# Performance work log

Hardware: AMD Instinct MI355X
Metric: run time of the kernel (lower is better)

Reference implementation:

```python
import jax, jax.numpy as jnp
import numpy as np

B, F, E, T = 4, 128, 3000, 6000  # batch, features, input edges, unroll_target


def setup_inputs() -> dict:
    key = jax.random.key(0)
    k1, k2 = jax.random.split(key)
    features = jax.random.normal(k1, (B, F, E), dtype=jnp.float32)
    # Sparse one-hot-like group matrix: each padded group matrix is binary with
    # a few nonzeros per target column (as produced by mesh.get_groups + pad_groups).
    unroll_mat = (jax.random.uniform(k2, (B, E, T)) < (2.0 / E)).astype(jnp.float32)
    # occurrences[b, t] = number of times target edge t occurs across groups;
    # pad_occurrences pads with 1, so clamp to a minimum of 1.
    occurrences = jnp.maximum(unroll_mat.sum(axis=1), 1.0)  # (B, T)
    return {"features": features, "unroll_mat": unroll_mat, "occurrences": occurrences}


def reference(features, unroll_mat, occurrences):
    # unroll_mat: (B, E, T) padded group matrix; occurrences: (B, T)
    # normalized mapping, then dense bmm: (B,F,E) @ (B,E,T) -> (B,F,T)
    norm_mat = unroll_mat / occurrences[:, None, :]
    return jnp.einsum('bfe,bet->bft', features, norm_mat)
```

## Files before the change

kernel.cpp:

```cpp
#include <hip/hip_runtime.h>

#define B 4
#define F 128
#define E 3000
#define T 6000
#define BN 48
#define KSTEP 32
#define NKT 94
#define NTT 125
#define ESLOT 40

typedef float f32x4 __attribute__((ext_vector_type(4)));
typedef short bf16x8 __attribute__((ext_vector_type(8)));

static __device__ __forceinline__ unsigned short f32_bf16(float x) {
    unsigned u = __float_as_uint(x);
    u += 0x7FFFu + ((u >> 16) & 1u);
    return (unsigned short)(u >> 16);
}

__global__ __launch_bounds__(256) void build_afrag(const float* __restrict__ feat,
                                                   unsigned short* __restrict__ afrag) {
    const int gid = blockIdx.x * 256 + threadIdx.x;
    if (gid >= B * NKT * 8 * 64) return;
    const int lane = gid & 63;
    const int frag = gid >> 6;
    const int ft = frag & 7;
    const int kt = (frag >> 3) % NKT;
    const int b  = frag / (8 * NKT);
    const int m  = ft * 16 + (lane & 15);
    const int k0 = kt * 32 + (lane >> 4) * 8;
    const float* src = feat + ((size_t)b * F + m) * E;
    unsigned short v[8];
#pragma unroll
    for (int j = 0; j < 8; ++j) {
        const int k = k0 + j;
        v[j] = (k < E) ? f32_bf16(src[k]) : (unsigned short)0;
    }
    uint4 pack;
    pack.x = (unsigned)v[0] | ((unsigned)v[1] << 16);
    pack.y = (unsigned)v[2] | ((unsigned)v[3] << 16);
    pack.z = (unsigned)v[4] | ((unsigned)v[5] << 16);
    pack.w = (unsigned)v[6] | ((unsigned)v[7] << 16);
    *reinterpret_cast<uint4*>(afrag + (size_t)frag * 512 + lane * 8) = pack;
}

__global__ __launch_bounds__(256, 2) void unpool_mfma_ws(
        const float* __restrict__ unroll,
        const unsigned short* __restrict__ afrag,
        const float* __restrict__ occ,
        float* __restrict__ out) {
    __shared__ unsigned short ut[4][2][BN * ESLOT];
    __shared__ f32x4 red[2][3][3][64];

    const int nwg  = NTT * B;
    const int orig = blockIdx.x + gridDim.x * blockIdx.y;
    const int q = nwg / 8, r = nwg % 8;
    const int xcd = orig & 7, lin = orig >> 3;
    const int newid = (xcd < r ? xcd * (q + 1) : r * (q + 1) + (xcd - r) * q) + lin;
    const int tb = newid % NTT;
    const int b  = newid / NTT;
    const int t0 = tb * BN;

    const int tid  = threadIdx.x;
    const int lane = tid & 63;
    const int w    = tid >> 6;
    const int lrow = lane & 15;
    const int g    = lane >> 4;

    const float* ub = unroll + (size_t)b * E * T + t0;
    const unsigned short* ab = afrag + (size_t)b * NKT * 8 * 512;
    unsigned short (*myut)[BN * ESLOT] = ut[w];

    int e_l[6], t4_l[6];
#pragma unroll
    for (int j = 0; j < 6; ++j) {
        const int idx = lane + 64 * j;
        e_l[j]  = idx / 12;
        t4_l[j] = (idx % 12) * 4;
    }

    const int s0 = w * 23 + (w < 2 ? w : 2);
    const int ns = 23 + (w < 2 ? 1 : 0);

    f32x4 acc[8][3] = {};

#define ULOAD(DST, S)                                                                  \
    { _Pragma("unroll") for (int j = 0; j < 6; ++j) {                                  \
          const int e = (S) * KSTEP + e_l[j];                                          \
          DST[j] = (e < E) ? *reinterpret_cast<const float4*>(ub + (size_t)e * T + t4_l[j]) \
                           : make_float4(0.0f, 0.0f, 0.0f, 0.0f); } }

#define UWRITE(SRC, BUF)                                                               \
    { _Pragma("unroll") for (int j = 0; j < 6; ++j) {                                  \
          unsigned short* p = &myut[BUF][e_l[j]];                                      \
          p[(t4_l[j] + 0) * ESLOT] = (__float_as_uint(SRC[j].x) != 0u) ? 0x3F80u : 0u; \
          p[(t4_l[j] + 1) * ESLOT] = (__float_as_uint(SRC[j].y) != 0u) ? 0x3F80u : 0u; \
          p[(t4_l[j] + 2) * ESLOT] = (__float_as_uint(SRC[j].z) != 0u) ? 0x3F80u : 0u; \
          p[(t4_l[j] + 3) * ESLOT] = (__float_as_uint(SRC[j].w) != 0u) ? 0x3F80u : 0u; } }

#define STEP(S, BUF, UVOLD, UVNEW)                                                     \
    {                                                                                  \
        bf16x8 afr[8];                                                                 \
        const unsigned short* ap = ab + (size_t)(S) * 8 * 512 + lane * 8;              \
        _Pragma("unroll") for (int ft = 0; ft < 8; ++ft)                               \
            afr[ft] = *reinterpret_cast<const bf16x8*>(ap + ft * 512);                 \
        __builtin_amdgcn_sched_barrier(0);                                             \
        if ((S) + 2 < s0 + ns) ULOAD(UVNEW, (S) + 2);                                  \
        const bf16x8 bf0 = *reinterpret_cast<const bf16x8*>(&myut[BUF][(0 * 16 + lrow) * ESLOT + 8 * g]); \
        const bf16x8 bf1 = *reinterpret_cast<const bf16x8*>(&myut[BUF][(1 * 16 + lrow) * ESLOT + 8 * g]); \
        const bf16x8 bf2 = *reinterpret_cast<const bf16x8*>(&myut[BUF][(2 * 16 + lrow) * ESLOT + 8 * g]); \
        _Pragma("unroll") for (int ft = 0; ft < 8; ++ft) {                             \
            acc[ft][0] = __builtin_amdgcn_mfma_f32_16x16x32_bf16(afr[ft], bf0, acc[ft][0], 0, 0, 0); \
            acc[ft][1] = __builtin_amdgcn_mfma_f32_16x16x32_bf16(afr[ft], bf1, acc[ft][1], 0, 0, 0); \
            acc[ft][2] = __builtin_amdgcn_mfma_f32_16x16x32_bf16(afr[ft], bf2, acc[ft][2], 0, 0, 0); } \
        if ((S) + 1 < s0 + ns) UWRITE(UVOLD, (BUF) ^ 1);                               \
    }

    float4 uvA[6], uvB[6];
    ULOAD(uvA, s0);
    UWRITE(uvA, 0);
    if (ns > 1) ULOAD(uvA, s0 + 1);

    for (int i = 0; i < ns; i += 2) {
        STEP(s0 + i, 0, uvA, uvB);
        if (i + 1 < ns) STEP(s0 + i + 1, 1, uvB, uvA);
    }
#undef STEP
#undef UWRITE
#undef ULOAD

    float inv[3];
#pragma unroll
    for (int nt = 0; nt < 3; ++nt)
        inv[nt] = 1.0f / occ[b * T + t0 + nt * 16 + lrow];
    float* ob = out + (size_t)b * F * T;

#pragma unroll
    for (int p = 0; p < 4; ++p) {
        __syncthreads();
#pragma unroll
        for (int c = 0; c < 2; ++c) {
            const int ft = 2 * p + c;
            const int fw = 2 * c + (p & 1);
            if (w != fw) {
                const int slot = (w - fw + 4) % 4 - 1;
#pragma unroll
                for (int nt = 0; nt < 3; ++nt)
                    red[c][slot][nt][lane] = acc[ft][nt];
            }
        }
        __syncthreads();
#pragma unroll
        for (int c = 0; c < 2; ++c) {
            const int ft = 2 * p + c;
            const int fw = 2 * c + (p & 1);
            if (w == fw) {
#pragma unroll
                for (int nt = 0; nt < 3; ++nt) {
                    f32x4 v = acc[ft][nt];
#pragma unroll
                    for (int sI = 0; sI < 3; ++sI) v += red[c][sI][nt][lane];
                    const int t = t0 + nt * 16 + lrow;
#pragma unroll
                    for (int rr = 0; rr < 4; ++rr) {
                        const int f = ft * 16 + g * 4 + rr;
                        __builtin_nontemporal_store(v[rr] * inv[nt], ob + (size_t)f * T + t);
                    }
                }
            }
        }
    }
}

__global__ void unpool_dense_fallback(const float* __restrict__ features,
                                      const float* __restrict__ unroll,
                                      const float* __restrict__ occ,
                                      float* __restrict__ out) {
    const int b = blockIdx.z;
    const int f = blockIdx.y;
    const int t = blockIdx.x * 64 + threadIdx.x;
    if (t >= T) return;
    const float* frow = features + ((size_t)b * F + f) * E;
    const float* ubp = unroll + (size_t)b * E * T;
    float acc = 0.0f;
    for (int e = 0; e < E; ++e) acc += frow[e] * ubp[(size_t)e * T + t];
    out[((size_t)b * F + f) * T + t] = acc / occ[b * T + t];
}

extern "C" void kernel_launch(void* const* d_in, const int* in_sizes, int n_in,
                              void* d_out, int out_size, void* d_ws, size_t ws_size,
                              hipStream_t stream) {
    const float* features = (const float*)d_in[0];
    const float* unroll   = (const float*)d_in[1];
    const float* occ      = (const float*)d_in[2];
    float* out = (float*)d_out;

    const size_t afrag_bytes = (size_t)B * NKT * 8 * 512 * sizeof(unsigned short);
    if (ws_size < afrag_bytes) {
        dim3 g((T + 63) / 64, F, B);
        unpool_dense_fallback<<<g, 64, 0, stream>>>(features, unroll, occ, out);
        return;
    }

    unsigned short* afrag = (unsigned short*)d_ws;

    const int nthr = B * NKT * 8 * 64;
    build_afrag<<<(nthr + 255) / 256, 256, 0, stream>>>(features, afrag);

    unpool_mfma_ws<<<dim3(NTT, B), 256, 0, stream>>>(unroll, afrag, occ, out);
}
```

Measured before the change: 74.90 us.

## Bit-pack unroll matrix in a pre-pass and expand bits to bf16 in the GEMM

Adds a pre-pass kernel that reads the full fp32 unroll matrix once and writes it as 64-bit ballot bitmasks, one bit per entry. The main MFMA kernel then reads these compact bitmasks instead of fp32 data and rebuilds the bf16 B fragments in registers by shifting and masking. This drops the LDS staging buffers and the transpose writes. The full 288MB fp32 read still happens, now in the separate bitpack kernel, so the gain depends on that streaming pass running near full bandwidth. It also adds a kernel launch and scattered 4-byte bitmask gathers in the GEMM.

```diff
diff --git a/kernel.cpp b/kernel.cpp
--- a/kernel.cpp
+++ b/kernel.cpp
@@ -8,7 +8,8 @@
 #define KSTEP 32
 #define NKT 94
 #define NTT 125
-#define ESLOT 40
+#define RQW 96
+#define RDW 192
 
 typedef float f32x4 __attribute__((ext_vector_type(4)));
 typedef short bf16x8 __attribute__((ext_vector_type(8)));
@@ -45,19 +46,43 @@
     *reinterpret_cast<uint4*>(afrag + (size_t)frag * 512 + lane * 8) = pack;
 }
 
-__global__ __launch_bounds__(256, 2) void unpool_mfma_ws(
-        const float* __restrict__ unroll,
+__global__ __launch_bounds__(256) void bitpack(const float* __restrict__ unroll,
+                                               unsigned long long* __restrict__ bitmask) {
+    const int rid  = blockIdx.x * 4 + (threadIdx.x >> 6);
+    const int lane = threadIdx.x & 63;
+    const float* row = unroll + (size_t)rid * T;
+    unsigned long long* orow = bitmask + (size_t)rid * RQW;
+
+#pragma unroll
+    for (int ch = 0; ch < 24; ++ch) {
+        float4 v = make_float4(0.0f, 0.0f, 0.0f, 0.0f);
+        if (ch < 23 || lane < 28)
+            v = *reinterpret_cast<const float4*>(row + ch * 256 + lane * 4);
+        const unsigned long long b0 = __ballot(v.x != 0.0f);
+        const unsigned long long b1 = __ballot(v.y != 0.0f);
+        const unsigned long long b2 = __ballot(v.z != 0.0f);
+        const unsigned long long b3 = __ballot(v.w != 0.0f);
+        if (lane == 0) {
+            orow[ch * 4 + 0] = b0;
+            orow[ch * 4 + 1] = b1;
+            orow[ch * 4 + 2] = b2;
+            orow[ch * 4 + 3] = b3;
+        }
+    }
+}
+
+__global__ __launch_bounds__(256, 2) void unpool_mfma_bits(
+        const unsigned* __restrict__ bm,
         const unsigned short* __restrict__ afrag,
         const float* __restrict__ occ,
         float* __restrict__ out) {
-    __shared__ unsigned short ut[4][2][BN * ESLOT];
     __shared__ f32x4 red[2][3][3][64];
 
     const int nwg  = NTT * B;
     const int orig = blockIdx.x + gridDim.x * blockIdx.y;
-    const int q = nwg / 8, r = nwg % 8;
+    const int q_ = nwg / 8, r_ = nwg % 8;
     const int xcd = orig & 7, lin = orig >> 3;
-    const int newid = (xcd < r ? xcd * (q + 1) : r * (q + 1) + (xcd - r) * q) + lin;
+    const int newid = (xcd < r_ ? xcd * (q_ + 1) : r_ * (q_ + 1) + (xcd - r_) * q_) + lin;
     const int tb = newid % NTT;
     const int b  = newid / NTT;
     const int t0 = tb * BN;
@@ -68,67 +93,59 @@
     const int lrow = lane & 15;
     const int g    = lane >> 4;
 
-    const float* ub = unroll + (size_t)b * E * T + t0;
     const unsigned short* ab = afrag + (size_t)b * NKT * 8 * 512;
-    unsigned short (*myut)[BN * ESLOT] = ut[w];
-
-    int e_l[6], t4_l[6];
-#pragma unroll
-    for (int j = 0; j < 6; ++j) {
-        const int idx = lane + 64 * j;
-        e_l[j]  = idx / 12;
-        t4_l[j] = (idx % 12) * 4;
+    const unsigned* bmb = bm + (size_t)b * E * RDW;
+
+    int C[3], sh[3];
+#pragma unroll
+    for (int nt = 0; nt < 3; ++nt) {
+        const int t = t0 + nt * 16 + lrow;
+        C[nt]  = (t >> 8) * 8 + (t & 3) * 2 + ((t >> 7) & 1);
+        sh[nt] = (t >> 2) & 31;
     }
 
     const int s0 = w * 23 + (w < 2 ? w : 2);
-    const int ns = 23 + (w < 2 ? 1 : 0);
+    const int send = s0 + 23 + (w < 2 ? 1 : 0);
 
     f32x4 acc[8][3] = {};
 
-#define ULOAD(DST, S)                                                                  \
-    { _Pragma("unroll") for (int j = 0; j < 6; ++j) {                                  \
-          const int e = (S) * KSTEP + e_l[j];                                          \
-          DST[j] = (e < E) ? *reinterpret_cast<const float4*>(ub + (size_t)e * T + t4_l[j]) \
-                           : make_float4(0.0f, 0.0f, 0.0f, 0.0f); } }
-
-#define UWRITE(SRC, BUF)                                                               \
-    { _Pragma("unroll") for (int j = 0; j < 6; ++j) {                                  \
-          unsigned short* p = &myut[BUF][e_l[j]];                                      \
-          p[(t4_l[j] + 0) * ESLOT] = (__float_as_uint(SRC[j].x) != 0u) ? 0x3F80u : 0u; \
-          p[(t4_l[j] + 1) * ESLOT] = (__float_as_uint(SRC[j].y) != 0u) ? 0x3F80u : 0u; \
-          p[(t4_l[j] + 2) * ESLOT] = (__float_as_uint(SRC[j].z) != 0u) ? 0x3F80u : 0u; \
-          p[(t4_l[j] + 3) * ESLOT] = (__float_as_uint(SRC[j].w) != 0u) ? 0x3F80u : 0u; } }
-
-#define STEP(S, BUF, UVOLD, UVNEW)                                                     \
-    {                                                                                  \
-        bf16x8 afr[8];                                                                 \
-        const unsigned short* ap = ab + (size_t)(S) * 8 * 512 + lane * 8;              \
-        _Pragma("unroll") for (int ft = 0; ft < 8; ++ft)                               \
-            afr[ft] = *reinterpret_cast<const bf16x8*>(ap + ft * 512);                 \
-        __builtin_amdgcn_sched_barrier(0);                                             \
-        if ((S) + 2 < s0 + ns) ULOAD(UVNEW, (S) + 2);                                  \
-        const bf16x8 bf0 = *reinterpret_cast<const bf16x8*>(&myut[BUF][(0 * 16 + lrow) * ESLOT + 8 * g]); \
-        const bf16x8 bf1 = *reinterpret_cast<const bf16x8*>(&myut[BUF][(1 * 16 + lrow) * ESLOT + 8 * g]); \
-        const bf16x8 bf2 = *reinterpret_cast<const bf16x8*>(&myut[BUF][(2 * 16 + lrow) * ESLOT + 8 * g]); \
-        _Pragma("unroll") for (int ft = 0; ft < 8; ++ft) {                             \
-            acc[ft][0] = __builtin_amdgcn_mfma_f32_16x16x32_bf16(afr[ft], bf0, acc[ft][0], 0, 0, 0); \
-            acc[ft][1] = __builtin_amdgcn_mfma_f32_16x16x32_bf16(afr[ft], bf1, acc[ft][1], 0, 0, 0); \
-            acc[ft][2] = __builtin_amdgcn_mfma_f32_16x16x32_bf16(afr[ft], bf2, acc[ft][2], 0, 0, 0); } \
-        if ((S) + 1 < s0 + ns) UWRITE(UVOLD, (BUF) ^ 1);                               \
-    }
-
-    float4 uvA[6], uvB[6];
-    ULOAD(uvA, s0);
-    UWRITE(uvA, 0);
-    if (ns > 1) ULOAD(uvA, s0 + 1);
-
-    for (int i = 0; i < ns; i += 2) {
-        STEP(s0 + i, 0, uvA, uvB);
-        if (i + 1 < ns) STEP(s0 + i + 1, 1, uvB, uvA);
-    }
-#undef STEP
-#undef UWRITE
-#undef ULOAD
+    for (int s = s0; s < send; ++s) {
+        unsigned q[3][8];
+        const unsigned* rp = bmb + (size_t)(32 * s + 8 * g) * RDW;
+#pragma unroll
+        for (int nt = 0; nt < 3; ++nt)
+#pragma unroll
+            for (int j = 0; j < 8; ++j)
+                q[nt][j] = rp[j * RDW + C[nt]];
+
+        bf16x8 afr[8];
+        const unsigned short* ap = ab + (size_t)s * 8 * 512 + lane * 8;
+#pragma unroll
+        for (int ft = 0; ft < 8; ++ft)
+            afr[ft] = *reinterpret_cast<const bf16x8*>(ap + ft * 512);
+
+        bf16x8 bf[3];
+#pragma unroll
+        for (int nt = 0; nt < 3; ++nt) {
+            union { uint4 u; bf16x8 v; } bu;
+            unsigned d[4];
+#pragma unroll
+            for (int m = 0; m < 4; ++m) {
+                const unsigned lo = (q[nt][2 * m]     >> sh[nt]) & 1u;
+                const unsigned hi = (q[nt][2 * m + 1] >> sh[nt]) & 1u;
+                d[m] = (lo ? 0x3F80u : 0u) | (hi ? 0x3F800000u : 0u);
+            }
+            bu.u.x = d[0]; bu.u.y = d[1]; bu.u.z = d[2]; bu.u.w = d[3];
+            bf[nt] = bu.v;
+        }
+
+#pragma unroll
+        for (int ft = 0; ft < 8; ++ft) {
+            acc[ft][0] = __builtin_amdgcn_mfma_f32_16x16x32_bf16(afr[ft], bf[0], acc[ft][0], 0, 0, 0);
+            acc[ft][1] = __builtin_amdgcn_mfma_f32_16x16x32_bf16(afr[ft], bf[1], acc[ft][1], 0, 0, 0);
+            acc[ft][2] = __builtin_amdgcn_mfma_f32_16x16x32_bf16(afr[ft], bf[2], acc[ft][2], 0, 0, 0);
+        }
+    }
 
     float inv[3];
 #pragma unroll
@@ -197,16 +214,22 @@
     float* out = (float*)d_out;
 
     const size_t afrag_bytes = (size_t)B * NKT * 8 * 512 * sizeof(unsigned short);
-    if (ws_size < afrag_bytes) {
+    const size_t bm_bytes    = (size_t)B * E * RQW * sizeof(unsigned long long);
+    if (ws_size < afrag_bytes + bm_bytes + 8192) {
         dim3 g((T + 63) / 64, F, B);
         unpool_dense_fallback<<<g, 64, 0, stream>>>(features, unroll, occ, out);
         return;
     }
 
     unsigned short* afrag = (unsigned short*)d_ws;
+    unsigned long long* bitmask =
+        (unsigned long long*)((char*)d_ws + afrag_bytes);
 
     const int nthr = B * NKT * 8 * 64;
     build_afrag<<<(nthr + 255) / 256, 256, 0, stream>>>(features, afrag);
 
-    unpool_mfma_ws<<<dim3(NTT, B), 256, 0, stream>>>(unroll, afrag, occ, out);
-}
+    bitpack<<<(B * E) / 4, 256, 0, stream>>>(unroll, bitmask);
+
+    unpool_mfma_bits<<<dim3(NTT, B), 256, 0, stream>>>(
+        (const unsigned*)bitmask, afrag, occ, out);
+}
```

Result: slower. 126.7 us (+69.2%).
